# Kernel optimization log

Hardware: AMD Instinct MI355X
Metric: run time of the kernel (lower is better)

The kernel has to match this reference:

```python
import jax, jax.numpy as jnp
import numpy as np
from jax import lax

B, T, D = 4, 4096, 1024
H = 16                 # n_heads
HD = D // H            # head_dim = 64
NS = 64                # num_slots
SPH = NS // H          # slots_per_head = 4
KPH = 2                # effective per-head top_k = min(max(2, 32//16), 4) = 2
K = KPH * H            # total topk width = 32
HM = 4096              # hidden_mlp


def _p(key, shape, scale=0.02):
    return jax.random.normal(key, shape, dtype=jnp.float32) * scale


def setup_inputs() -> dict:
    key = jax.random.key(0)
    ks = jax.random.split(key, 24)
    return {
        "x": jax.random.normal(ks[0], (B, T, D), dtype=jnp.float32),
        "slot_init": _p(ks[1], (H, SPH, HD)),
        # route_mlp: Linear(2D, D) -> GELU -> Linear(D, NS); weights stored [in, out]
        "rw1": _p(ks[2], (2 * D, D)), "rb1": jnp.zeros((D,), jnp.float32),
        "rw2": _p(ks[3], (D, NS)), "rb2": jnp.zeros((NS,), jnp.float32),
        # GRUCell(HD, HD): torch layout [3*HD, HD]
        "gwi": _p(ks[4], (3 * HD, HD), 0.1), "gwh": _p(ks[5], (3 * HD, HD), 0.1),
        "gbi": jnp.zeros((3 * HD,), jnp.float32), "gbh": jnp.zeros((3 * HD,), jnp.float32),
        # slot_hidden_proj: Linear(HD, 4*HD); slot_out_head: Linear(4*HD, HD)
        "hpw": _p(ks[6], (HD, 4 * HD)), "hpb": jnp.zeros((4 * HD,), jnp.float32),
        "ohw": _p(ks[7], (4 * HD, HD)), "ohb": jnp.zeros((HD,), jnp.float32),
        # slot_value_proj: Linear(D, HM); slot_value_out: Linear(HM, D)
        "vpw": _p(ks[8], (D, HM)), "vpb": jnp.zeros((HM,), jnp.float32),
        "vow": _p(ks[9], (HM, D)), "vob": jnp.zeros((D,), jnp.float32),
        # out_proj: Linear(D, D)
        "opw": _p(ks[10], (D, D)), "opb": jnp.zeros((D,), jnp.float32),
        "tau": jnp.ones((1,), jnp.float32),
    }


def _gelu(x):
    return jax.nn.gelu(x, approximate=False)


def _forward(x, slot_init, rw1, rb1, rw2, rb2, gwi, gwh, gbi, gbh,
             hpw, hpb, ohw, ohb, vpw, vpb, vow, vob, opw, opb, tau):
    # ---- routing ----
    S0 = slot_init.reshape(NS, HD)                     # [NS, HD]
    slot_mean = S0.mean(axis=0)                        # [HD]
    slot_mean_full = jnp.tile(slot_mean, H)            # [D]
    ctx = jnp.concatenate(
        [x, jnp.broadcast_to(slot_mean_full, (B, T, D))], axis=-1)  # [B,T,2D]
    h1 = _gelu(ctx @ rw1 + rb1)
    route_logits = (h1 @ rw2 + rb2) / (jnp.abs(tau[0]) + 0.1)       # [B,T,NS]

    topk_vals, topk_idx = lax.top_k(route_logits, K)   # [B,T,K]
    topk_w = jax.nn.softmax(topk_vals, axis=-1)
    bi = jnp.arange(B)[:, None, None]
    ti = jnp.arange(T)[None, :, None]
    alpha = jnp.zeros((B, T, NS), x.dtype).at[bi, ti, topk_idx].set(topk_w)

    # ---- per-head slot pooling (vectorized over heads) ----
    alpha_h = alpha.reshape(B, T, H, SPH)              # [B,T,H,S]
    x_heads = x.reshape(B, T, H, HD)                   # [B,T,H,HD]
    slot_input = jnp.einsum('bths,bthd->bhsd', alpha_h, x_heads)   # [B,H,S,HD]
    wsum = alpha_h.sum(axis=1) + 1e-8                  # [B,H,S]
    slot_in = slot_input / wsum[..., None]

    # ---- GRU cell update (torch GRUCell semantics) ----
    h_prev = jnp.broadcast_to(slot_init[None], (B, H, SPH, HD))
    gi = slot_in @ gwi.T + gbi                         # [B,H,S,3HD]
    gh = h_prev @ gwh.T + gbh
    ir, iz, in_ = jnp.split(gi, 3, axis=-1)
    hr, hz, hn = jnp.split(gh, 3, axis=-1)
    r = jax.nn.sigmoid(ir + hr)
    z = jax.nn.sigmoid(iz + hz)
    n = jnp.tanh(in_ + r * hn)
    h_new = (1.0 - z) * n + z * h_prev                 # [B,H,S,HD]

    S_new = _gelu(h_new @ hpw + hpb) @ ohw + ohb       # [B,H,S,HD]

    # ---- broadcast back to tokens ----
    out = jnp.einsum('bths,bhsd->bthd', alpha_h, S_new).reshape(B, T, D)
    out = _gelu(out @ vpw + vpb) @ vow + vob
    out = out @ opw + opb
    return out


def reference(x, slot_init, rw1, rb1, rw2, rb2, gwi, gwh, gbi, gbh,
              hpw, hpb, ohw, ohb, vpw, vpb, vow, vob, opw, opb, tau):
    return _forward(x, slot_init, rw1, rb1, rw2, rb2, gwi, gwh, gbi, gbh,
                    hpw, hpb, ohw, ohb, vpw, vpb, vow, vob, opw, opb, tau)
```

## Files before the change

kernel.cpp:

```cpp
#include <hip/hip_runtime.h>
#include <cstddef>
#include <cstdint>

#define Bb 4
#define Tt 4096
#define Dd 1024
#define Hh 16
#define HDd 64
#define NSs 64
#define SPHh 4
#define HMm 4096
#define MTOK (Bb*Tt)

typedef _Float16 f16x8 __attribute__((ext_vector_type(8)));
typedef _Float16 f16x4 __attribute__((ext_vector_type(4)));
typedef float f32x4 __attribute__((ext_vector_type(4)));

__device__ __forceinline__ float gelu_f(float x) {
    return 0.5f * x * (1.0f + erff(x * 0.70710678118654752440f));
}

__device__ __forceinline__ int xcd_swz(int nwg) {
    int orig = blockIdx.y * gridDim.x + blockIdx.x;
    int cpx = nwg >> 3;
    return (orig & 7) * cpx + (orig >> 3);
}

__global__ __launch_bounds__(256) void cb_part_k(const float* __restrict__ slot_init,
                                                 const float* __restrict__ rw1,
                                                 float* __restrict__ cbp) {
    __shared__ float sm[64];
    int tid = threadIdx.x;
    if (tid < 64) {
        float s = 0.f;
        for (int i = 0; i < 64; ++i) s += slot_init[i * 64 + tid];
        sm[tid] = s * (1.0f / 64.0f);
    }
    __syncthreads();
    int j = blockIdx.x * 256 + tid;
    int k0 = blockIdx.y * 64;
    float acc = 0.f;
#pragma unroll 8
    for (int k = 0; k < 64; ++k)
        acc = fmaf(sm[k], rw1[(size_t)(1024 + k0 + k) * 1024 + j], acc);
    cbp[(size_t)blockIdx.y * 1024 + j] = acc;
}

__global__ __launch_bounds__(256) void cb_comb_k(const float* __restrict__ cbp,
                                                 float* __restrict__ cb) {
    int j = blockIdx.x * 256 + threadIdx.x;
    float acc = 0.f;
#pragma unroll
    for (int c = 0; c < 16; ++c) acc += cbp[(size_t)c * 1024 + j];
    cb[j] = acc;
}

__global__ __launch_bounds__(256) void wsplitT_k(const float* __restrict__ rw1,
                                                 _Float16* __restrict__ whiT,
                                                 _Float16* __restrict__ wloT) {
    __shared__ float t[32][33];
    int n0 = blockIdx.x * 32, k0 = blockIdx.y * 32;
    int tx = threadIdx.x & 31, ty = threadIdx.x >> 5;
#pragma unroll
    for (int i = 0; i < 32; i += 8)
        t[ty + i][tx] = rw1[(size_t)(k0 + ty + i) * 1024 + n0 + tx];
    __syncthreads();
#pragma unroll
    for (int i = 0; i < 32; i += 8) {
        float v = t[tx][ty + i];
        _Float16 h = (_Float16)v;
        _Float16 l = (_Float16)(v - (float)h);
        whiT[(size_t)(n0 + ty + i) * 1024 + k0 + tx] = h;
        wloT[(size_t)(n0 + ty + i) * 1024 + k0 + tx] = l;
    }
}

__global__ __launch_bounds__(256) void xsplit_k(const float* __restrict__ x,
                                                _Float16* __restrict__ xhi,
                                                _Float16* __restrict__ xlo) {
    size_t i = ((size_t)blockIdx.x * 256 + threadIdx.x) * 8;
    float4 a = *(const float4*)(x + i);
    float4 b = *(const float4*)(x + i + 4);
    float v[8] = {a.x, a.y, a.z, a.w, b.x, b.y, b.z, b.w};
    f16x8 h, l;
#pragma unroll
    for (int j = 0; j < 8; ++j) {
        _Float16 hv = (_Float16)v[j];
        h[j] = hv;
        l[j] = (_Float16)(v[j] - (float)hv);
    }
    *(f16x8*)(xhi + i) = h;
    *(f16x8*)(xlo + i) = l;
}

__global__ __launch_bounds__(512, 2) void hgemm4p_k(const _Float16* __restrict__ Ah,
                                                    const _Float16* __restrict__ Al,
                                                    const _Float16* __restrict__ Bh,
                                                    const _Float16* __restrict__ Bl,
                                                    const float* __restrict__ bias1,
                                                    const float* __restrict__ bias2,
                                                    float* __restrict__ C,
                                                    int M, int N, int K) {
    __shared__ __align__(16) _Float16 Ahs[2][256][32];
    __shared__ __align__(16) _Float16 Als[2][256][32];
    __shared__ __align__(16) _Float16 Bhs[2][256][32];
    __shared__ __align__(16) _Float16 Bls[2][256][32];
    const int tid = threadIdx.x;
    const int wid = tid >> 6;
    const int lane = tid & 63;
    const int swz = xcd_swz(gridDim.x * gridDim.y);
    const int brow = (swz / gridDim.x) * 256;
    const int bcol = (swz % gridDim.x) * 256;
    const int wm = wid >> 2;
    const int wn = wid & 3;

    const int srow = lane >> 2;
    const int scol = ((lane & 3) ^ ((lane >> 3) & 3)) * 8;
    const int fr = lane & 15;
    const int fkp = (((lane >> 4) ^ ((lane >> 1) & 3))) * 8;
    const int crow = (lane >> 4) * 4;

    const int nk = K >> 5;

    f32x4 acc[8][4];
#pragma unroll
    for (int m = 0; m < 8; ++m)
#pragma unroll
        for (int n = 0; n < 4; ++n)
            acc[m][n] = f32x4{0.f, 0.f, 0.f, 0.f};

    auto stage = [&](int t) {
        const int slot = t & 1;
        const size_t kk = (size_t)t << 5;
#pragma unroll
        for (int i = 0; i < 2; ++i) {
            int r0 = wid * 32 + i * 16;
            const _Float16* gah = Ah + (size_t)(brow + r0 + srow) * K + kk + scol;
            __builtin_amdgcn_global_load_lds(
                (const __attribute__((address_space(1))) void*)gah,
                (__attribute__((address_space(3))) void*)&Ahs[slot][r0][0], 16, 0, 0);
            const _Float16* gal = Al + (size_t)(brow + r0 + srow) * K + kk + scol;
            __builtin_amdgcn_global_load_lds(
                (const __attribute__((address_space(1))) void*)gal,
                (__attribute__((address_space(3))) void*)&Als[slot][r0][0], 16, 0, 0);
            const _Float16* gbh = Bh + (size_t)(bcol + r0 + srow) * K + kk + scol;
            __builtin_amdgcn_global_load_lds(
                (const __attribute__((address_space(1))) void*)gbh,
                (__attribute__((address_space(3))) void*)&Bhs[slot][r0][0], 16, 0, 0);
            const _Float16* gbl = Bl + (size_t)(bcol + r0 + srow) * K + kk + scol;
            __builtin_amdgcn_global_load_lds(
                (const __attribute__((address_space(1))) void*)gbl,
                (__attribute__((address_space(3))) void*)&Bls[slot][r0][0], 16, 0, 0);
        }
    };

    stage(0);
    if (nk > 1) stage(1);

    for (int t = 0; t < nk; ++t) {
        if (t + 1 < nk) asm volatile("s_waitcnt vmcnt(8)" ::: "memory");
        else            asm volatile("s_waitcnt vmcnt(0)" ::: "memory");
        __builtin_amdgcn_sched_barrier(0);
        __builtin_amdgcn_s_barrier();
        __builtin_amdgcn_sched_barrier(0);

        const int slot = t & 1;
        f16x8 afh[4], afl[4], bfh[4], bfl[4];
#pragma unroll
        for (int m = 0; m < 4; ++m) {
            afh[m] = *(const f16x8*)&Ahs[slot][wm * 128 + m * 16 + fr][fkp];
            afl[m] = *(const f16x8*)&Als[slot][wm * 128 + m * 16 + fr][fkp];
        }
#pragma unroll
        for (int n = 0; n < 2; ++n) {
            bfh[n] = *(const f16x8*)&Bhs[slot][wn * 64 + n * 16 + fr][fkp];
            bfl[n] = *(const f16x8*)&Bls[slot][wn * 64 + n * 16 + fr][fkp];
        }
        __builtin_amdgcn_sched_barrier(0);
        __builtin_amdgcn_s_barrier();
        asm volatile("s_waitcnt lgkmcnt(0)" ::: "memory");
        __builtin_amdgcn_sched_barrier(0);
        __builtin_amdgcn_s_setprio(1);
#pragma unroll
        for (int m = 0; m < 4; ++m)
#pragma unroll
            for (int n = 0; n < 2; ++n) {
                acc[m][n] = __builtin_amdgcn_mfma_f32_16x16x32_f16(afl[m], bfh[n], acc[m][n], 0, 0, 0);
                acc[m][n] = __builtin_amdgcn_mfma_f32_16x16x32_f16(afh[m], bfl[n], acc[m][n], 0, 0, 0);
                acc[m][n] = __builtin_amdgcn_mfma_f32_16x16x32_f16(afh[m], bfh[n], acc[m][n], 0, 0, 0);
            }
        __builtin_amdgcn_s_setprio(0);
        __builtin_amdgcn_sched_barrier(0);
#pragma unroll
        for (int n = 2; n < 4; ++n) {
            bfh[n] = *(const f16x8*)&Bhs[slot][wn * 64 + n * 16 + fr][fkp];
            bfl[n] = *(const f16x8*)&Bls[slot][wn * 64 + n * 16 + fr][fkp];
        }
        __builtin_amdgcn_sched_barrier(0);
        __builtin_amdgcn_s_barrier();
        asm volatile("s_waitcnt lgkmcnt(0)" ::: "memory");
        __builtin_amdgcn_sched_barrier(0);
        __builtin_amdgcn_s_setprio(1);
#pragma unroll
        for (int m = 0; m < 4; ++m)
#pragma unroll
            for (int n = 2; n < 4; ++n) {
                acc[m][n] = __builtin_amdgcn_mfma_f32_16x16x32_f16(afl[m], bfh[n], acc[m][n], 0, 0, 0);
                acc[m][n] = __builtin_amdgcn_mfma_f32_16x16x32_f16(afh[m], bfl[n], acc[m][n], 0, 0, 0);
                acc[m][n] = __builtin_amdgcn_mfma_f32_16x16x32_f16(afh[m], bfh[n], acc[m][n], 0, 0, 0);
            }
        __builtin_amdgcn_s_setprio(0);
        __builtin_amdgcn_sched_barrier(0);
#pragma unroll
        for (int m = 0; m < 4; ++m) {
            afh[m] = *(const f16x8*)&Ahs[slot][wm * 128 + (m + 4) * 16 + fr][fkp];
            afl[m] = *(const f16x8*)&Als[slot][wm * 128 + (m + 4) * 16 + fr][fkp];
        }
        __builtin_amdgcn_sched_barrier(0);
        __builtin_amdgcn_s_barrier();
        asm volatile("s_waitcnt lgkmcnt(0)" ::: "memory");
        __builtin_amdgcn_sched_barrier(0);
        __builtin_amdgcn_s_setprio(1);
#pragma unroll
        for (int m = 0; m < 4; ++m)
#pragma unroll
            for (int n = 0; n < 2; ++n) {
                acc[m + 4][n] = __builtin_amdgcn_mfma_f32_16x16x32_f16(afl[m], bfh[n], acc[m + 4][n], 0, 0, 0);
                acc[m + 4][n] = __builtin_amdgcn_mfma_f32_16x16x32_f16(afh[m], bfl[n], acc[m + 4][n], 0, 0, 0);
                acc[m + 4][n] = __builtin_amdgcn_mfma_f32_16x16x32_f16(afh[m], bfh[n], acc[m + 4][n], 0, 0, 0);
            }
        __builtin_amdgcn_s_setprio(0);
        __builtin_amdgcn_sched_barrier(0);
        __builtin_amdgcn_s_barrier();
        __builtin_amdgcn_sched_barrier(0);
        if (t + 2 < nk) stage(t + 2);
        __builtin_amdgcn_s_setprio(1);
#pragma unroll
        for (int m = 0; m < 4; ++m)
#pragma unroll
            for (int n = 2; n < 4; ++n) {
                acc[m + 4][n] = __builtin_amdgcn_mfma_f32_16x16x32_f16(afl[m], bfh[n], acc[m + 4][n], 0, 0, 0);
                acc[m + 4][n] = __builtin_amdgcn_mfma_f32_16x16x32_f16(afh[m], bfl[n], acc[m + 4][n], 0, 0, 0);
                acc[m + 4][n] = __builtin_amdgcn_mfma_f32_16x16x32_f16(afh[m], bfh[n], acc[m + 4][n], 0, 0, 0);
            }
        __builtin_amdgcn_s_setprio(0);
        __builtin_amdgcn_sched_barrier(0);
    }

#pragma unroll
    for (int m = 0; m < 8; ++m) {
        int row0 = brow + wm * 128 + m * 16 + crow;
#pragma unroll
        for (int n = 0; n < 4; ++n) {
            int col = bcol + wn * 64 + n * 16 + fr;
            float bv = bias1[col] + bias2[col];
#pragma unroll
            for (int r = 0; r < 4; ++r) {
                float v = acc[m][n][r] + bv;
                C[(size_t)(row0 + r) * N + col] = gelu_f(v);
            }
        }
    }
    (void)M;
}

__global__ __launch_bounds__(256) void logits2_k(const float* __restrict__ A,
                                                 const float* __restrict__ Bw,
                                                 const float* __restrict__ rb2,
                                                 const float* __restrict__ taup,
                                                 float* __restrict__ Cl) {
    __shared__ float At[16][68];
    __shared__ float Bs[16][64];
    const int tid = threadIdx.x;
    const int m0 = blockIdx.x * 64;
    const int rg = tid >> 4;
    const int cg = tid & 15;
    const int srow = tid >> 2;
    const int skk  = (tid & 3) * 4;
    const int bk = tid >> 4;
    const int bc = (tid & 15) * 4;

    float acc[4][4] = {};

    float4 av = *(const float4*)(A + (size_t)(m0 + srow) * 1024 + skk);
    float4 bv = *(const float4*)(Bw + (size_t)bk * 64 + bc);

    for (int k0 = 0; k0 < 1024; k0 += 16) {
        __syncthreads();
        At[skk + 0][srow] = av.x;
        At[skk + 1][srow] = av.y;
        At[skk + 2][srow] = av.z;
        At[skk + 3][srow] = av.w;
        *(float4*)&Bs[bk][bc] = bv;
        __syncthreads();
        if (k0 + 16 < 1024) {
            av = *(const float4*)(A + (size_t)(m0 + srow) * 1024 + k0 + 16 + skk);
            bv = *(const float4*)(Bw + (size_t)(k0 + 16 + bk) * 64 + bc);
        }
#pragma unroll
        for (int k = 0; k < 16; ++k) {
            float4 a4 = *(const float4*)&At[k][rg * 4];
            float4 b4 = *(const float4*)&Bs[k][cg * 4];
            float a[4] = {a4.x, a4.y, a4.z, a4.w};
            float b[4] = {b4.x, b4.y, b4.z, b4.w};
#pragma unroll
            for (int i = 0; i < 4; ++i)
#pragma unroll
                for (int j = 0; j < 4; ++j)
                    acc[i][j] = fmaf(a[i], b[j], acc[i][j]);
        }
    }
    float inv = 1.0f / (fabsf(taup[0]) + 0.1f);
#pragma unroll
    for (int i = 0; i < 4; ++i)
#pragma unroll
        for (int j = 0; j < 4; ++j)
            Cl[(size_t)(m0 + rg * 4 + i) * 64 + cg * 4 + j] =
                (acc[i][j] + rb2[cg * 4 + j]) * inv;
}

__global__ __launch_bounds__(256) void topk_k(const float* __restrict__ logits,
                                              float* __restrict__ alpha,
                                              _Float16* __restrict__ alpha16) {
    int wave = threadIdx.x >> 6;
    int lane = threadIdx.x & 63;
    int t = blockIdx.x * 4 + wave;
    float li = logits[(size_t)t * 64 + lane];
    float m = li;
#pragma unroll
    for (int off = 32; off; off >>= 1) m = fmaxf(m, __shfl_xor(m, off, 64));
    int cnt = 0;
    for (int off = 1; off < 64; ++off) {
        int j = (lane + off) & 63;
        float lj = __shfl(li, j, 64);
        cnt += (lj > li) || (lj == li && j < lane);
    }
    float e = (cnt < 32) ? expf(li - m) : 0.0f;
    float s = e;
#pragma unroll
    for (int off = 32; off; off >>= 1) s += __shfl_xor(s, off, 64);
    float a = e / s;
    alpha[(size_t)t * 64 + lane] = a;
    alpha16[(size_t)t * 64 + lane] = (_Float16)a;
}

__global__ __launch_bounds__(256) void pool_part_k(const float* __restrict__ x,
                                                   const float* __restrict__ alpha,
                                                   float* __restrict__ part,
                                                   float* __restrict__ partw) {
    int bh = blockIdx.x;
    int c = blockIdx.y;
    int b = bh >> 4, h = bh & 15;
    int tid = threadIdx.x;
    int s = tid >> 6, d = tid & 63;
    __shared__ float lx[16][64];
    __shared__ float la[16][4];
    float acc = 0.f, wacc = 0.f;
    const int tchunk = Tt / 8;
    const int t0base = c * tchunk;
    for (int t0 = 0; t0 < tchunk; t0 += 16) {
        int ttr = tid >> 4;
        int ddr = (tid & 15) * 4;
        size_t trow = (size_t)b * Tt + t0base + t0 + ttr;
        float4 xv = *(const float4*)(x + trow * Dd + h * 64 + ddr);
        *(float4*)&lx[ttr][ddr] = xv;
        if (tid < 64) {
            int tt2 = tid >> 2, ss = tid & 3;
            la[tt2][ss] = alpha[((size_t)b * Tt + t0base + t0 + tt2) * 64 + h * 4 + ss];
        }
        __syncthreads();
#pragma unroll
        for (int q = 0; q < 16; ++q) {
            float av = la[q][s];
            acc = fmaf(av, lx[q][d], acc);
            wacc += av;
        }
        __syncthreads();
    }
    part[(((size_t)c * 64 + bh) * 4 + s) * 64 + d] = acc;
    if (d == 0) partw[((size_t)c * 64 + bh) * 4 + s] = wacc;
}

__global__ __launch_bounds__(256) void pool_comb_k(const float* __restrict__ part,
                                                   const float* __restrict__ partw,
                                                   float* __restrict__ slot_in) {
    int bh = blockIdx.x;
    int tid = threadIdx.x;
    int s = tid >> 6, d = tid & 63;
    float acc = 0.f, w = 0.f;
    for (int c = 0; c < 8; ++c) {
        acc += part[(((size_t)c * 64 + bh) * 4 + s) * 64 + d];
        w   += partw[((size_t)c * 64 + bh) * 4 + s];
    }
    slot_in[((size_t)bh * 4 + s) * 64 + d] = acc / (w + 1e-8f);
}

__global__ __launch_bounds__(64) void gru_k(const float* __restrict__ slot_in,
                                            const float* __restrict__ slot_init,
                                            const float* __restrict__ gwi,
                                            const float* __restrict__ gwh,
                                            const float* __restrict__ gbi,
                                            const float* __restrict__ gbh,
                                            const float* __restrict__ hpw,
                                            const float* __restrict__ hpb,
                                            const float* __restrict__ ohw,
                                            const float* __restrict__ ohb,
                                            float* __restrict__ S_new) {
    int slot = blockIdx.x;
    int hs = slot & 63;
    int d = threadIdx.x;
    __shared__ float si[64], hp[64], hn[64], g[256];
    si[d] = slot_in[(size_t)slot * 64 + d];
    hp[d] = slot_init[(size_t)hs * 64 + d];
    __syncthreads();
    float gi_r = gbi[d], gi_z = gbi[64 + d], gi_n = gbi[128 + d];
    float gh_r = gbh[d], gh_z = gbh[64 + d], gh_n = gbh[128 + d];
    for (int k = 0; k < 64; ++k) {
        float sv = si[k], hv = hp[k];
        gi_r = fmaf(sv, gwi[(size_t)(d) * 64 + k], gi_r);
        gi_z = fmaf(sv, gwi[(size_t)(64 + d) * 64 + k], gi_z);
        gi_n = fmaf(sv, gwi[(size_t)(128 + d) * 64 + k], gi_n);
        gh_r = fmaf(hv, gwh[(size_t)(d) * 64 + k], gh_r);
        gh_z = fmaf(hv, gwh[(size_t)(64 + d) * 64 + k], gh_z);
        gh_n = fmaf(hv, gwh[(size_t)(128 + d) * 64 + k], gh_n);
    }
    float r = 1.0f / (1.0f + expf(-(gi_r + gh_r)));
    float z = 1.0f / (1.0f + expf(-(gi_z + gh_z)));
    float n = tanhf(gi_n + r * gh_n);
    float hnew = (1.0f - z) * n + z * hp[d];
    hn[d] = hnew;
    __syncthreads();
    float p0 = hpb[d], p1 = hpb[64 + d], p2 = hpb[128 + d], p3 = hpb[192 + d];
    for (int k = 0; k < 64; ++k) {
        float hv = hn[k];
        p0 = fmaf(hv, hpw[(size_t)k * 256 + d], p0);
        p1 = fmaf(hv, hpw[(size_t)k * 256 + 64 + d], p1);
        p2 = fmaf(hv, hpw[(size_t)k * 256 + 128 + d], p2);
        p3 = fmaf(hv, hpw[(size_t)k * 256 + 192 + d], p3);
    }
    g[d] = gelu_f(p0); g[64 + d] = gelu_f(p1); g[128 + d] = gelu_f(p2); g[192 + d] = gelu_f(p3);
    __syncthreads();
    float o = ohb[d];
    for (int j = 0; j < 256; ++j) o = fmaf(g[j], ohw[(size_t)j * 64 + d], o);
    S_new[(size_t)slot * 64 + d] = o;
}

__global__ __launch_bounds__(256) void pmat_k(const float* __restrict__ Snew,
                                              const float* __restrict__ vpw,
                                              _Float16* __restrict__ PT) {
    const int h = blockIdx.y;
    const int tid = threadIdx.x;
    const int j = blockIdx.x * 256 + tid;
    __shared__ float S[16][64];
    for (int i = tid; i < 1024; i += 256) {
        int row = i >> 6, d = i & 63;
        int b = row >> 2, s = row & 3;
        S[row][d] = Snew[((size_t)b * 64 + h * 4 + s) * 64 + d];
    }
    __syncthreads();
    float acc[16];
#pragma unroll
    for (int r = 0; r < 16; ++r) acc[r] = 0.f;
    const float* wp = vpw + (size_t)h * 64 * HMm + j;
#pragma unroll 4
    for (int d = 0; d < 64; ++d) {
        float w = wp[(size_t)d * HMm];
#pragma unroll
        for (int r = 0; r < 16; ++r) acc[r] = fmaf(S[r][d], w, acc[r]);
    }
#pragma unroll
    for (int b = 0; b < 4; ++b) {
        f16x4 o;
#pragma unroll
        for (int s = 0; s < 4; ++s) o[s] = (_Float16)acc[b * 4 + s];
        *(f16x4*)&PT[((size_t)b * HMm + j) * 64 + h * 4] = o;
    }
}

__global__ __launch_bounds__(256) void transp_f16_k(const float* __restrict__ in,
                                                    _Float16* __restrict__ out,
                                                    int K, int N) {
    __shared__ float t[32][33];
    int n0 = blockIdx.x * 32, k0 = blockIdx.y * 32;
    int tx = threadIdx.x & 31, ty = threadIdx.x >> 5;
#pragma unroll
    for (int i = 0; i < 32; i += 8)
        t[ty + i][tx] = in[(size_t)(k0 + ty + i) * N + n0 + tx];
    __syncthreads();
#pragma unroll
    for (int i = 0; i < 32; i += 8)
        out[(size_t)(n0 + ty + i) * K + k0 + tx] = (_Float16)t[tx][ty + i];
}

__global__ __launch_bounds__(256) void vgen_k(const _Float16* __restrict__ alpha16,
                                              const _Float16* __restrict__ PT,
                                              const float* __restrict__ vpb,
                                              _Float16* __restrict__ v1a,
                                              _Float16* __restrict__ v1b) {
    __shared__ __align__(16) _Float16 As[128][64];
    __shared__ __align__(16) _Float16 Bs[128][64];
    const int tid = threadIdx.x;
    const int wid = tid >> 6;
    const int lane = tid & 63;
    const int swz = xcd_swz(gridDim.x * gridDim.y);
    const int brow = (swz / gridDim.x) * 128;
    const int bcol = (swz % gridDim.x) * 128;
    const int b = brow >> 12;
    const _Float16* Bt = PT + (size_t)b * HMm * 64;
    _Float16* Cb = (brow < 8192) ? v1a : v1b;
    const int rowoff = (brow < 8192) ? brow : brow - 8192;
    const int wr = (wid >> 1) * 64;
    const int wc = (wid & 1) * 64;

    f32x4 acc[4][4];
#pragma unroll
    for (int m = 0; m < 4; ++m)
#pragma unroll
        for (int n = 0; n < 4; ++n)
            acc[m][n] = f32x4{0.f, 0.f, 0.f, 0.f};

    const int lrow = lane >> 3;
    const int lcol = (lane & 7) * 8;
    const int fr = lane & 15;
    const int fk = (lane >> 4) * 8;

#pragma unroll
    for (int i = 0; i < 4; ++i) {
        int seg = wid * 4 + i;
        const _Float16* g = alpha16 + (size_t)(brow + seg * 8 + lrow) * 64 + lcol;
        __builtin_amdgcn_global_load_lds(
            (const __attribute__((address_space(1))) void*)g,
            (__attribute__((address_space(3))) void*)&As[seg * 8][0], 16, 0, 0);
    }
#pragma unroll
    for (int i = 0; i < 4; ++i) {
        int seg = wid * 4 + i;
        const _Float16* g = Bt + (size_t)(bcol + seg * 8 + lrow) * 64 + lcol;
        __builtin_amdgcn_global_load_lds(
            (const __attribute__((address_space(1))) void*)g,
            (__attribute__((address_space(3))) void*)&Bs[seg * 8][0], 16, 0, 0);
    }
    __syncthreads();
#pragma unroll
    for (int kb = 0; kb < 2; ++kb) {
        f16x8 af[4], bf[4];
#pragma unroll
        for (int m = 0; m < 4; ++m)
            af[m] = *(const f16x8*)&As[wr + m * 16 + fr][kb * 32 + fk];
#pragma unroll
        for (int n = 0; n < 4; ++n)
            bf[n] = *(const f16x8*)&Bs[wc + n * 16 + fr][kb * 32 + fk];
#pragma unroll
        for (int m = 0; m < 4; ++m)
#pragma unroll
            for (int n = 0; n < 4; ++n)
                acc[m][n] = __builtin_amdgcn_mfma_f32_16x16x32_f16(af[m], bf[n], acc[m][n], 0, 0, 0);
    }

    const int crow = (lane >> 4) * 4;
#pragma unroll
    for (int m = 0; m < 4; ++m) {
        int row0 = rowoff + wr + m * 16 + crow;
#pragma unroll
        for (int n = 0; n < 4; ++n) {
            int col = bcol + wc + n * 16 + fr;
            float bv = vpb[col];
#pragma unroll
            for (int r = 0; r < 4; ++r) {
                float v = acc[m][n][r] + bv;
                Cb[(size_t)(row0 + r) * HMm + col] = (_Float16)gelu_f(v);
            }
        }
    }
}

template <int OUT_F16>
__global__ __launch_bounds__(512, 2) void hgemm8_k(const _Float16* __restrict__ A0,
                                                   const _Float16* __restrict__ A1,
                                                   int splitrow,
                                                   const _Float16* __restrict__ Bt,
                                                   const float* __restrict__ bias,
                                                   void* __restrict__ Cv,
                                                   int M, int N, int K) {
    __shared__ __align__(16) _Float16 As[2][256][64];
    __shared__ __align__(16) _Float16 Bs[2][256][64];
    const int tid = threadIdx.x;
    const int wid = tid >> 6;
    const int lane = tid & 63;
    const int swz = xcd_swz(gridDim.x * gridDim.y);
    const int brow = (swz / gridDim.x) * 256;
    const int bcol = (swz % gridDim.x) * 256;
    const _Float16* Ab = (brow < splitrow) ? A0 : A1;
    const int arow0 = brow - ((brow < splitrow) ? 0 : splitrow);
    const int wm = wid >> 2;
    const int wn = wid & 3;

    const int srow = lane >> 3;
    const int scol = ((lane & 7) ^ (lane >> 3)) * 8;
    const int fr = lane & 15;
    const int fk0 = (((lane >> 4) ^ (lane & 7))) * 8;
    const int fk1 = (((4 + (lane >> 4)) ^ (lane & 7))) * 8;
    const int crow = (lane >> 4) * 4;

    const int nk = K >> 6;

    f32x4 acc[8][4];
#pragma unroll
    for (int m = 0; m < 8; ++m)
#pragma unroll
        for (int n = 0; n < 4; ++n)
            acc[m][n] = f32x4{0.f, 0.f, 0.f, 0.f};

    auto stage = [&](int t) {
        const int slot = t & 1;
        const size_t kk = (size_t)t << 6;
#pragma unroll
        for (int j = 0; j < 4; ++j) {
            const _Float16* ga = Ab + (size_t)(arow0 + j * 64 + wid * 8 + srow) * K + kk + scol;
            __builtin_amdgcn_global_load_lds(
                (const __attribute__((address_space(1))) void*)ga,
                (__attribute__((address_space(3))) void*)&As[slot][j * 64 + wid * 8][0], 16, 0, 0);
        }
#pragma unroll
        for (int j = 0; j < 4; ++j) {
            const _Float16* gb = Bt + (size_t)(bcol + j * 64 + wid * 8 + srow) * K + kk + scol;
            __builtin_amdgcn_global_load_lds(
                (const __attribute__((address_space(1))) void*)gb,
                (__attribute__((address_space(3))) void*)&Bs[slot][j * 64 + wid * 8][0], 16, 0, 0);
        }
    };

    stage(0);
    stage(1);

    for (int t = 0; t < nk; ++t) {
        if (t + 1 < nk) asm volatile("s_waitcnt vmcnt(8)" ::: "memory");
        else            asm volatile("s_waitcnt vmcnt(0)" ::: "memory");
        __builtin_amdgcn_sched_barrier(0);
        __builtin_amdgcn_s_barrier();
        __builtin_amdgcn_sched_barrier(0);

        const int slot = t & 1;
        f16x8 af[4][2], bf[4][2];
#pragma unroll
        for (int m = 0; m < 4; ++m) {
            af[m][0] = *(const f16x8*)&As[slot][wm * 128 + m * 16 + fr][fk0];
            af[m][1] = *(const f16x8*)&As[slot][wm * 128 + m * 16 + fr][fk1];
        }
#pragma unroll
        for (int n = 0; n < 2; ++n) {
            bf[n][0] = *(const f16x8*)&Bs[slot][wn * 64 + n * 16 + fr][fk0];
            bf[n][1] = *(const f16x8*)&Bs[slot][wn * 64 + n * 16 + fr][fk1];
        }
        __builtin_amdgcn_sched_barrier(0);
        __builtin_amdgcn_s_barrier();
        asm volatile("s_waitcnt lgkmcnt(0)" ::: "memory");
        __builtin_amdgcn_sched_barrier(0);
        __builtin_amdgcn_s_setprio(1);
#pragma unroll
        for (int m = 0; m < 4; ++m)
#pragma unroll
            for (int n = 0; n < 2; ++n)
#pragma unroll
                for (int kk = 0; kk < 2; ++kk)
                    acc[m][n] = __builtin_amdgcn_mfma_f32_16x16x32_f16(af[m][kk], bf[n][kk], acc[m][n], 0, 0, 0);
        __builtin_amdgcn_s_setprio(0);
        __builtin_amdgcn_sched_barrier(0);
#pragma unroll
        for (int n = 2; n < 4; ++n) {
            bf[n][0] = *(const f16x8*)&Bs[slot][wn * 64 + n * 16 + fr][fk0];
            bf[n][1] = *(const f16x8*)&Bs[slot][wn * 64 + n * 16 + fr][fk1];
        }
        __builtin_amdgcn_sched_barrier(0);
        __builtin_amdgcn_s_barrier();
        asm volatile("s_waitcnt lgkmcnt(0)" ::: "memory");
        __builtin_amdgcn_sched_barrier(0);
        __builtin_amdgcn_s_setprio(1);
#pragma unroll
        for (int m = 0; m < 4; ++m)
#pragma unroll
            for (int n = 2; n < 4; ++n)
#pragma unroll
                for (int kk = 0; kk < 2; ++kk)
                    acc[m][n] = __builtin_amdgcn_mfma_f32_16x16x32_f16(af[m][kk], bf[n][kk], acc[m][n], 0, 0, 0);
        __builtin_amdgcn_s_setprio(0);
        __builtin_amdgcn_sched_barrier(0);
#pragma unroll
        for (int m = 0; m < 4; ++m) {
            af[m][0] = *(const f16x8*)&As[slot][wm * 128 + (m + 4) * 16 + fr][fk0];
            af[m][1] = *(const f16x8*)&As[slot][wm * 128 + (m + 4) * 16 + fr][fk1];
        }
        __builtin_amdgcn_sched_barrier(0);
        __builtin_amdgcn_s_barrier();
        asm volatile("s_waitcnt lgkmcnt(0)" ::: "memory");
        __builtin_amdgcn_sched_barrier(0);
        __builtin_amdgcn_s_setprio(1);
#pragma unroll
        for (int m = 0; m < 4; ++m)
#pragma unroll
            for (int n = 0; n < 2; ++n)
#pragma unroll
                for (int kk = 0; kk < 2; ++kk)
                    acc[m + 4][n] = __builtin_amdgcn_mfma_f32_16x16x32_f16(af[m][kk], bf[n][kk], acc[m + 4][n], 0, 0, 0);
        __builtin_amdgcn_s_setprio(0);
        __builtin_amdgcn_sched_barrier(0);
        __builtin_amdgcn_s_barrier();
        __builtin_amdgcn_sched_barrier(0);
        if (t + 2 < nk) stage(t + 2);
        __builtin_amdgcn_s_setprio(1);
#pragma unroll
        for (int m = 0; m < 4; ++m)
#pragma unroll
            for (int n = 2; n < 4; ++n)
#pragma unroll
                for (int kk = 0; kk < 2; ++kk)
                    acc[m + 4][n] = __builtin_amdgcn_mfma_f32_16x16x32_f16(af[m][kk], bf[n][kk], acc[m + 4][n], 0, 0, 0);
        __builtin_amdgcn_s_setprio(0);
        __builtin_amdgcn_sched_barrier(0);
    }

#pragma unroll
    for (int m = 0; m < 8; ++m) {
        int row0 = brow + wm * 128 + m * 16 + crow;
#pragma unroll
        for (int n = 0; n < 4; ++n) {
            int col = bcol + wn * 64 + n * 16 + fr;
            float bv = bias[col];
#pragma unroll
            for (int r = 0; r < 4; ++r) {
                float v = acc[m][n][r] + bv;
                size_t idx = (size_t)(row0 + r) * N + col;
                if (OUT_F16) ((_Float16*)Cv)[idx] = (_Float16)v;
                else ((float*)Cv)[idx] = v;
            }
        }
    }
    (void)M;
}

extern "C" void kernel_launch(void* const* d_in, const int* in_sizes, int n_in,
                              void* d_out, int out_size, void* d_ws, size_t ws_size,
                              hipStream_t stream) {
    const float* x         = (const float*)d_in[0];
    const float* slot_init = (const float*)d_in[1];
    const float* rw1       = (const float*)d_in[2];
    const float* rb1       = (const float*)d_in[3];
    const float* rw2       = (const float*)d_in[4];
    const float* rb2       = (const float*)d_in[5];
    const float* gwi       = (const float*)d_in[6];
    const float* gwh       = (const float*)d_in[7];
    const float* gbi       = (const float*)d_in[8];
    const float* gbh       = (const float*)d_in[9];
    const float* hpw       = (const float*)d_in[10];
    const float* hpb       = (const float*)d_in[11];
    const float* ohw       = (const float*)d_in[12];
    const float* ohb       = (const float*)d_in[13];
    const float* vpw       = (const float*)d_in[14];
    const float* vpb       = (const float*)d_in[15];
    const float* vow       = (const float*)d_in[16];
    const float* vob       = (const float*)d_in[17];
    const float* opw       = (const float*)d_in[18];
    const float* opb       = (const float*)d_in[19];
    const float* tau       = (const float*)d_in[20];
    float* out = (float*)d_out;

    float* ws = (float*)d_ws;
    size_t off = 0;
    auto alloc = [&](size_t nfloats) { float* p = ws + off; off += (nfloats + 63) & ~(size_t)63; return p; };

    float* cb     = alloc(1024);
    float* cbp    = alloc(16 * 1024);
    float* h1     = alloc((size_t)MTOK * 1024);
    _Float16* v1a = (_Float16*)h1;
    float* logits = alloc((size_t)MTOK * 64);
    float* alpha  = alloc((size_t)MTOK * 64);
    _Float16* alpha16 = (_Float16*)alloc((size_t)MTOK * 64 / 2);
    float* slotin = alloc(256 * 64);
    float* part   = alloc((size_t)8 * 64 * 4 * 64);
    float* partw  = alloc(8 * 64 * 4);
    float* Snew   = alloc(256 * 64);
    _Float16* PT   = (_Float16*)alloc((size_t)Bb * HMm * 64 / 2);
    _Float16* vowT = (_Float16*)alloc((size_t)Dd * HMm / 2);
    _Float16* opwT = (_Float16*)alloc((size_t)Dd * Dd / 2);
    _Float16* v2f16 = (_Float16*)alloc((size_t)MTOK * Dd / 2);
    _Float16* w1hiT = (_Float16*)alloc((size_t)Dd * Dd / 2);
    _Float16* w1loT = (_Float16*)alloc((size_t)Dd * Dd / 2);

    _Float16* xhi = (_Float16*)d_out;
    _Float16* xlo = xhi + (size_t)MTOK * Dd;
    _Float16* v1b = (_Float16*)d_out;

    cb_part_k<<<dim3(4, 16), 256, 0, stream>>>(slot_init, rw1, cbp);
    cb_comb_k<<<4, 256, 0, stream>>>(cbp, cb);
    wsplitT_k<<<dim3(Dd / 32, Dd / 32), 256, 0, stream>>>(rw1, w1hiT, w1loT);
    xsplit_k<<<(MTOK * Dd) / (256 * 8), 256, 0, stream>>>(x, xhi, xlo);
    hgemm4p_k<<<dim3(Dd / 256, MTOK / 256), 512, 0, stream>>>(
        xhi, xlo, w1hiT, w1loT, rb1, cb, h1, MTOK, Dd, Dd);
    logits2_k<<<MTOK / 64, 256, 0, stream>>>(h1, rw2, rb2, tau, logits);
    topk_k<<<MTOK / 4, 256, 0, stream>>>(logits, alpha, alpha16);

    transp_f16_k<<<dim3(Dd / 32, HMm / 32), 256, 0, stream>>>(vow, vowT, HMm, Dd);
    transp_f16_k<<<dim3(Dd / 32, Dd / 32), 256, 0, stream>>>(opw, opwT, Dd, Dd);

    pool_part_k<<<dim3(64, 8), 256, 0, stream>>>(x, alpha, part, partw);
    pool_comb_k<<<64, 256, 0, stream>>>(part, partw, slotin);
    gru_k<<<256, 64, 0, stream>>>(slotin, slot_init, gwi, gwh, gbi, gbh,
                                  hpw, hpb, ohw, ohb, Snew);

    pmat_k<<<dim3(HMm / 256, Hh), 256, 0, stream>>>(Snew, vpw, PT);

    vgen_k<<<dim3(HMm / 128, MTOK / 128), 256, 0, stream>>>(
        alpha16, PT, vpb, v1a, v1b);
    hgemm8_k<1><<<dim3(Dd / 256, MTOK / 256), 512, 0, stream>>>(
        v1a, v1b, 8192, vowT, vob, v2f16, MTOK, Dd, HMm);
    hgemm8_k<0><<<dim3(Dd / 256, MTOK / 256), 512, 0, stream>>>(
        v2f16, v2f16, MTOK, opwT, opb, out, MTOK, Dd, Dd);

    (void)in_sizes; (void)n_in; (void)out_size; (void)ws_size;
}
```

Baseline: 500.7 us.

## Fuse routing logits with top-k softmax and pool from fp16 x

Merges the logits GEMM and the top-k masked softmax into one kernel. Logits are staged in shared memory, and each wave then processes 16 token rows, which removes the global logits buffer round trip and one launch. Slot pooling now reads the fp16 high half of the split x instead of fp32 x, halving that read traffic. The costs are less parallelism in the top-k phase (fewer blocks, serial rows per wave) and lower-precision pooled slot inputs.

```diff
diff --git a/kernel.cpp b/kernel.cpp
--- a/kernel.cpp
+++ b/kernel.cpp
@@ -264,13 +264,15 @@
     (void)M;
 }
 
-__global__ __launch_bounds__(256) void logits2_k(const float* __restrict__ A,
-                                                 const float* __restrict__ Bw,
-                                                 const float* __restrict__ rb2,
-                                                 const float* __restrict__ taup,
-                                                 float* __restrict__ Cl) {
+__global__ __launch_bounds__(256) void logtop_k(const float* __restrict__ A,
+                                                const float* __restrict__ Bw,
+                                                const float* __restrict__ rb2,
+                                                const float* __restrict__ taup,
+                                                float* __restrict__ alpha,
+                                                _Float16* __restrict__ alpha16) {
     __shared__ float At[16][68];
     __shared__ float Bs[16][64];
+    __shared__ float Lg[64][65];
     const int tid = threadIdx.x;
     const int m0 = blockIdx.x * 64;
     const int rg = tid >> 4;
@@ -315,36 +317,35 @@
     for (int i = 0; i < 4; ++i)
 #pragma unroll
         for (int j = 0; j < 4; ++j)
-            Cl[(size_t)(m0 + rg * 4 + i) * 64 + cg * 4 + j] =
-                (acc[i][j] + rb2[cg * 4 + j]) * inv;
-}
-
-__global__ __launch_bounds__(256) void topk_k(const float* __restrict__ logits,
-                                              float* __restrict__ alpha,
-                                              _Float16* __restrict__ alpha16) {
-    int wave = threadIdx.x >> 6;
-    int lane = threadIdx.x & 63;
-    int t = blockIdx.x * 4 + wave;
-    float li = logits[(size_t)t * 64 + lane];
-    float m = li;
-#pragma unroll
-    for (int off = 32; off; off >>= 1) m = fmaxf(m, __shfl_xor(m, off, 64));
-    int cnt = 0;
-    for (int off = 1; off < 64; ++off) {
-        int j = (lane + off) & 63;
-        float lj = __shfl(li, j, 64);
-        cnt += (lj > li) || (lj == li && j < lane);
-    }
-    float e = (cnt < 32) ? expf(li - m) : 0.0f;
-    float s = e;
-#pragma unroll
-    for (int off = 32; off; off >>= 1) s += __shfl_xor(s, off, 64);
-    float a = e / s;
-    alpha[(size_t)t * 64 + lane] = a;
-    alpha16[(size_t)t * 64 + lane] = (_Float16)a;
-}
-
-__global__ __launch_bounds__(256) void pool_part_k(const float* __restrict__ x,
+            Lg[rg * 4 + i][cg * 4 + j] = (acc[i][j] + rb2[cg * 4 + j]) * inv;
+    __syncthreads();
+
+    const int wave = tid >> 6;
+    const int lane = tid & 63;
+    const size_t tbase = (size_t)blockIdx.x * 64;
+    for (int tt = 0; tt < 16; ++tt) {
+        int row = wave * 16 + tt;
+        float li = Lg[row][lane];
+        float m = li;
+#pragma unroll
+        for (int off = 32; off; off >>= 1) m = fmaxf(m, __shfl_xor(m, off, 64));
+        int cnt = 0;
+        for (int off = 1; off < 64; ++off) {
+            int j = (lane + off) & 63;
+            float lj = __shfl(li, j, 64);
+            cnt += (lj > li) || (lj == li && j < lane);
+        }
+        float e = (cnt < 32) ? expf(li - m) : 0.0f;
+        float s = e;
+#pragma unroll
+        for (int off = 32; off; off >>= 1) s += __shfl_xor(s, off, 64);
+        float a = e / s;
+        alpha[(tbase + row) * 64 + lane] = a;
+        alpha16[(tbase + row) * 64 + lane] = (_Float16)a;
+    }
+}
+
+__global__ __launch_bounds__(256) void pool_part_k(const _Float16* __restrict__ xh,
                                                    const float* __restrict__ alpha,
                                                    float* __restrict__ part,
                                                    float* __restrict__ partw) {
@@ -362,8 +363,11 @@
         int ttr = tid >> 4;
         int ddr = (tid & 15) * 4;
         size_t trow = (size_t)b * Tt + t0base + t0 + ttr;
-        float4 xv = *(const float4*)(x + trow * Dd + h * 64 + ddr);
-        *(float4*)&lx[ttr][ddr] = xv;
+        f16x4 xv = *(const f16x4*)(xh + trow * Dd + h * 64 + ddr);
+        lx[ttr][ddr + 0] = (float)xv[0];
+        lx[ttr][ddr + 1] = (float)xv[1];
+        lx[ttr][ddr + 2] = (float)xv[2];
+        lx[ttr][ddr + 3] = (float)xv[3];
         if (tid < 64) {
             int tt2 = tid >> 2, ss = tid & 3;
             la[tt2][ss] = alpha[((size_t)b * Tt + t0base + t0 + tt2) * 64 + h * 4 + ss];
@@ -772,7 +776,6 @@
     float* cbp    = alloc(16 * 1024);
     float* h1     = alloc((size_t)MTOK * 1024);
     _Float16* v1a = (_Float16*)h1;
-    float* logits = alloc((size_t)MTOK * 64);
     float* alpha  = alloc((size_t)MTOK * 64);
     _Float16* alpha16 = (_Float16*)alloc((size_t)MTOK * 64 / 2);
     float* slotin = alloc(256 * 64);
@@ -796,13 +799,12 @@
     xsplit_k<<<(MTOK * Dd) / (256 * 8), 256, 0, stream>>>(x, xhi, xlo);
     hgemm4p_k<<<dim3(Dd / 256, MTOK / 256), 512, 0, stream>>>(
         xhi, xlo, w1hiT, w1loT, rb1, cb, h1, MTOK, Dd, Dd);
-    logits2_k<<<MTOK / 64, 256, 0, stream>>>(h1, rw2, rb2, tau, logits);
-    topk_k<<<MTOK / 4, 256, 0, stream>>>(logits, alpha, alpha16);
+    logtop_k<<<MTOK / 64, 256, 0, stream>>>(h1, rw2, rb2, tau, alpha, alpha16);
 
     transp_f16_k<<<dim3(Dd / 32, HMm / 32), 256, 0, stream>>>(vow, vowT, HMm, Dd);
     transp_f16_k<<<dim3(Dd / 32, Dd / 32), 256, 0, stream>>>(opw, opwT, Dd, Dd);
 
-    pool_part_k<<<dim3(64, 8), 256, 0, stream>>>(x, alpha, part, partw);
+    pool_part_k<<<dim3(64, 8), 256, 0, stream>>>(xhi, alpha, part, partw);
     pool_comb_k<<<64, 256, 0, stream>>>(part, partw, slotin);
     gru_k<<<256, 64, 0, stream>>>(slotin, slot_init, gwi, gwh, gbi, gbh,
                                   hpw, hpb, ohw, ohb, Snew);
```

Measured after the change: 527.6 us. 5.4% more time.
